# Kernel tuning notes

Hardware: AMD Instinct MI355X
Metric: run time of the kernel (lower is better)

The kernel has to match this reference:

```python
import jax, jax.numpy as jnp
import numpy as np
import math

HIDDEN = 384
HEADS = 4
HEAD_DIM = HIDDEN // HEADS
B, T = 8, 2048


def _shift_rel(pos_tensor):
    # pos_tensor: [b, h, t, 2t-1] -> [b, h, t, t] (Transformer-XL shift trick)
    b, h, t, n = pos_tensor.shape
    zero_pad = jnp.zeros((b, h, t, 1), dtype=pos_tensor.dtype)
    padded = jnp.concatenate([zero_pad, pos_tensor], axis=-1)  # [b,h,t,n+1]
    padded = padded.reshape(b, h, n + 1, t)
    shifted = padded[:, :, 1:].reshape(b, h, t, n)
    return shifted[:, :, :, : n // 2 + 1]  # [b,h,t,t]


def setup_inputs() -> dict:
    key = jax.random.key(0)
    ks = jax.random.split(key, 12)
    s = 1.0 / math.sqrt(HIDDEN)
    inp = {
        "hidden_states": jax.random.normal(ks[0], (B, T, HIDDEN), jnp.float32),
        "pos_emb": jax.random.normal(ks[1], (1, 2 * T - 1, HIDDEN), jnp.float32),
        "attention_mask": jnp.ones((B, 1, T), jnp.int32),
        "Wq": jax.random.normal(ks[2], (HIDDEN, HIDDEN), jnp.float32) * s,
        "bq": jnp.zeros((HIDDEN,), jnp.float32),
        "Wk": jax.random.normal(ks[3], (HIDDEN, HIDDEN), jnp.float32) * s,
        "bk": jnp.zeros((HIDDEN,), jnp.float32),
        "Wv": jax.random.normal(ks[4], (HIDDEN, HIDDEN), jnp.float32) * s,
        "bv": jnp.zeros((HIDDEN,), jnp.float32),
        "Wo": jax.random.normal(ks[5], (HIDDEN, HIDDEN), jnp.float32) * s,
        "bo": jnp.zeros((HIDDEN,), jnp.float32),
        "Wpos": jax.random.normal(ks[6], (HIDDEN, HIDDEN), jnp.float32) * s,
        "pos_bias_u": jax.random.normal(ks[7], (HEADS, HEAD_DIM), jnp.float32) * s,
        "pos_bias_v": jax.random.normal(ks[8], (HEADS, HEAD_DIM), jnp.float32) * s,
    }
    return inp


def reference(hidden_states, pos_emb, attention_mask, Wq, bq, Wk, bk, Wv, bv,
              Wo, bo, Wpos, pos_bias_u, pos_bias_v):
    bsz, q_len, _ = hidden_states.shape
    # projections (nn.Linear applies x @ W.T + b; weights here stored as [in, out])
    q = (hidden_states @ Wq + bq).reshape(bsz, q_len, HEADS, HEAD_DIM)
    k = (hidden_states @ Wk + bk).reshape(bsz, q_len, HEADS, HEAD_DIM)
    v = (hidden_states @ Wv + bv).reshape(bsz, q_len, HEADS, HEAD_DIM)
    pos = (pos_emb @ Wpos).reshape(pos_emb.shape[0], -1, HEADS, HEAD_DIM)

    q_u = (q + pos_bias_u).transpose(0, 2, 1, 3)  # [b,h,t,d]
    q_v = (q + pos_bias_v).transpose(0, 2, 1, 3)

    # content score: [b,h,t,t]
    matrix_ac = jnp.einsum('bhqd,bkhd->bhqk', q_u, k)
    # position score: [b,h,t,2t-1] then shift
    matrix_bd = jnp.einsum('bhqd,pnhd->bhqn', q_v, pos)
    matrix_bd = _shift_rel(matrix_bd)

    scores = (matrix_ac + matrix_bd) / math.sqrt(HEAD_DIM)

    mask = (attention_mask[:, None] == 0)  # [b,1,1,t]
    min_val = jnp.finfo(scores.dtype).min
    scores = jnp.where(mask, min_val, scores)
    attn = jax.nn.softmax(scores, axis=-1)
    attn = jnp.where(mask, 0.0, attn)

    out = jnp.einsum('bhqk,bkhd->bqhd', attn, v).reshape(bsz, q_len, HIDDEN)
    return out @ Wo + bo
```

## Files before the change

### kernel.cpp

```cpp
#include <hip/hip_runtime.h>
#include <hip/hip_bf16.h>

#define TSEQ 2048
#define HID 384
#define NHEAD 4
#define HD 96
#define NBATCH 8

using bf16 = __bf16;
typedef bf16 bf16x8 __attribute__((ext_vector_type(8)));
typedef bf16 bf16x4 __attribute__((ext_vector_type(4)));
typedef float f32x4 __attribute__((ext_vector_type(4)));
typedef unsigned long long u64;

static __device__ __forceinline__ f32x4 mfma16(bf16x8 a, bf16x8 b, f32x4 c) {
    return __builtin_amdgcn_mfma_f32_16x16x32_bf16(a, b, c, 0, 0, 0);
}

#define LDS_HANDOFF()                                   \
    __builtin_amdgcn_sched_barrier(0x7F);               \
    asm volatile("s_waitcnt lgkmcnt(0)");               \
    __builtin_amdgcn_sched_barrier(0x7F)

#define GL2LDS(g, l) __builtin_amdgcn_global_load_lds(                        \
    (const __attribute__((address_space(1))) unsigned int*)(const void*)(g),  \
    (__attribute__((address_space(3))) unsigned int*)(void*)(l), 16, 0, 0)

__global__ void k_conv8m(const float* __restrict__ hs, bf16* __restrict__ dhs,
                         const float* __restrict__ pe, bf16* __restrict__ dpe) {
    int blk = blockIdx.x;
    const float* src; bf16* dst; int t; int n8;
    if (blk < 3072) { src = hs; dst = dhs; t = blk * 256 + threadIdx.x; n8 = 786432; }
    else            { src = pe; dst = dpe; t = (blk - 3072) * 256 + threadIdx.x; n8 = 196560; }
    if (t >= n8) return;
    const float4* s4 = reinterpret_cast<const float4*>(src);
    float4 a = s4[2 * t], b = s4[2 * t + 1];
    bf16x8 o;
    o[0] = (bf16)a.x; o[1] = (bf16)a.y; o[2] = (bf16)a.z; o[3] = (bf16)a.w;
    o[4] = (bf16)b.x; o[5] = (bf16)b.y; o[6] = (bf16)b.z; o[7] = (bf16)b.w;
    *reinterpret_cast<bf16x8*>(dst + 8 * t) = o;
}

__global__ void k_convT5(const float* __restrict__ W0, const float* __restrict__ W1,
                         const float* __restrict__ W2, const float* __restrict__ W3,
                         const float* __restrict__ W4,
                         bf16* __restrict__ T0, bf16* __restrict__ T1,
                         bf16* __restrict__ T2, bf16* __restrict__ T3,
                         bf16* __restrict__ T4) {
    int t = blockIdx.x * 256 + threadIdx.x;
    int which = blockIdx.y;
    const float* W = (which == 0) ? W0 : (which == 1) ? W1 : (which == 2) ? W2
                     : (which == 3) ? W3 : W4;
    bf16* T = (which == 0) ? T0 : (which == 1) ? T1 : (which == 2) ? T2
              : (which == 3) ? T3 : T4;
    int n = t / HID, k = t % HID;
    T[t] = (bf16)W[(size_t)k * HID + n];
}

__launch_bounds__(256, 2)
__global__ void k_proj(const bf16* __restrict__ X, const bf16* __restrict__ P,
                       const bf16* __restrict__ wqT, const bf16* __restrict__ wkT,
                       const bf16* __restrict__ wvT, const bf16* __restrict__ wpT,
                       const float* __restrict__ bq, const float* __restrict__ bk,
                       const float* __restrict__ bv,
                       const float* __restrict__ pbu, const float* __restrict__ pbv,
                       bf16* __restrict__ qu, bf16* __restrict__ qv,
                       bf16* __restrict__ kws, bf16* __restrict__ vt,
                       bf16* __restrict__ pp) {
    __shared__ bf16 wt_lds[96][392];
    const float SC = 0.14724450f;
    int mat = blockIdx.z;
    int m0 = blockIdx.x * 64;
    if (mat == 3 && m0 >= 4095) return;
    int n0 = blockIdx.y * 96;
    const bf16* A  = (mat == 3) ? P : X;
    const bf16* WT = (mat == 0) ? wqT : (mat == 1) ? wkT : (mat == 2) ? wvT : wpT;
    int tid = threadIdx.x;
    #pragma unroll
    for (int s = 0; s < 18; ++s) {
        int cc = tid + 256 * s;
        int r = cc / 48, ch = cc % 48;
        *reinterpret_cast<int4*>(&wt_lds[r][ch * 8]) =
            *reinterpret_cast<const int4*>(WT + (size_t)(n0 + r) * HID + ch * 8);
    }
    __syncthreads();
    int lane = tid & 63, w = tid >> 6;
    int c = lane & 15, g = lane >> 4;
    int arow = m0 + 16 * w + c;
    if (mat == 3 && arow > 4095) arow = 4095;
    const bf16* Abase = A + (size_t)arow * HID + 8 * g;
    f32x4 acc[6] = {};
    for (int ks = 0; ks < 12; ++ks) {
        bf16x8 a = *reinterpret_cast<const bf16x8*>(Abase + 32 * ks);
        #pragma unroll
        for (int jt = 0; jt < 6; ++jt) {
            bf16x8 b = *reinterpret_cast<const bf16x8*>(&wt_lds[16 * jt + c][32 * ks + 8 * g]);
            acc[jt] = mfma16(a, b, acc[jt]);
        }
    }
    int h = blockIdx.y;
    int rbase = m0 + 16 * w + 4 * g;
    if (mat == 0) {
        #pragma unroll
        for (int jt = 0; jt < 6; ++jt) {
            int n = n0 + 16 * jt + c;
            int d = 16 * jt + c;
            float bb = bq[n], bu = pbu[n], bvv = pbv[n];
            #pragma unroll
            for (int j = 0; j < 4; ++j) {
                int m = rbase + j;
                int b_ = m >> 11, t = m & 2047;
                size_t o = (((size_t)(b_ * NHEAD + h)) * TSEQ + t) * HD + d;
                float q = acc[jt][j] + bb;
                qu[o] = (bf16)((q + bu) * SC);
                qv[o] = (bf16)((q + bvv) * SC);
            }
        }
    } else if (mat == 1) {
        #pragma unroll
        for (int jt = 0; jt < 6; ++jt) {
            int n = n0 + 16 * jt + c;
            int d = 16 * jt + c;
            float bb = bk[n];
            #pragma unroll
            for (int j = 0; j < 4; ++j) {
                int m = rbase + j;
                int b_ = m >> 11, t = m & 2047;
                size_t o = (((size_t)(b_ * NHEAD + h)) * TSEQ + t) * HD + d;
                kws[o] = (bf16)(acc[jt][j] + bb);
            }
        }
    } else if (mat == 2) {
        #pragma unroll
        for (int jt = 0; jt < 6; ++jt) {
            int d = 16 * jt + c;
            float bb = bv[n0 + 16 * jt + c];
            int m = rbase;
            int b_ = m >> 11, t0 = m & 2047;
            size_t o = (((size_t)(b_ * NHEAD + h)) * HD + d) * TSEQ + t0;
            bf16x4 pk;
            #pragma unroll
            for (int j = 0; j < 4; ++j) pk[j] = (bf16)(acc[jt][j] + bb);
            *reinterpret_cast<bf16x4*>(vt + o) = pk;
        }
    } else {
        #pragma unroll
        for (int jt = 0; jt < 6; ++jt) {
            int d = 16 * jt + c;
            #pragma unroll
            for (int j = 0; j < 4; ++j) {
                int m = rbase + j;
                if (m < 4095) {
                    size_t o = ((size_t)h * 4096 + m) * HD + d;
                    pp[o] = (bf16)acc[jt][j];
                }
            }
        }
    }
}

__launch_bounds__(256, 2)
__global__ void k_attn(const bf16* __restrict__ qu, const bf16* __restrict__ qv,
                       const bf16* __restrict__ kws, const bf16* __restrict__ vt,
                       const bf16* __restrict__ pp, const int* __restrict__ mask,
                       bf16* __restrict__ out) {
    __shared__ bf16 k_lds[128][104];
    __shared__ bf16 vt_lds[96][128];
    __shared__ bf16 wp_lds[4][16][168];

    int bid = blockIdx.x;
    int x = bid & 7, j5 = bid >> 3;
    int h = x & 3;
    int b_ = (x >> 2) * 4 + (j5 >> 5);
    int qb = j5 & 31;
    int bh = b_ * NHEAD + h;
    int q0 = qb * 64;

    int tid = threadIdx.x, lane = tid & 63, w = tid >> 6;
    int c = lane & 15, g = lane >> 4;
    const int NB = 2032 - q0 - 16 * w;

    bf16* k_flat = &k_lds[0][0];
    bf16* vt_flat = &vt_lds[0][0];
    int cc0 = tid, cc1 = tid + 256, cc2 = tid + 512, cc3 = tid + 768;
    int cc4 = tid + 1024, cc5 = tid + 1280, cc6 = tid + 1536;
    int kr0 = cc0 / 13, kc0 = cc0 % 13;  int kO0 = kr0 * HD + (kc0 == 12 ? 0 : kc0 * 8);
    int kr1 = cc1 / 13, kc1 = cc1 % 13;  int kO1 = kr1 * HD + (kc1 == 12 ? 0 : kc1 * 8);
    int kr2 = cc2 / 13, kc2 = cc2 % 13;  int kO2 = kr2 * HD + (kc2 == 12 ? 0 : kc2 * 8);
    int kr3 = cc3 / 13, kc3 = cc3 % 13;  int kO3 = kr3 * HD + (kc3 == 12 ? 0 : kc3 * 8);
    int kr4 = cc4 / 13, kc4 = cc4 % 13;  int kO4 = kr4 * HD + (kc4 == 12 ? 0 : kc4 * 8);
    int kr5 = cc5 / 13, kc5 = cc5 % 13;  int kO5 = kr5 * HD + (kc5 == 12 ? 0 : kc5 * 8);
    int kr6 = cc6 / 13, kc6 = cc6 % 13;  int kO6 = kr6 * HD + (kc6 == 12 ? 0 : kc6 * 8);
    bf16* kL0 = k_flat + (size_t)(64 * w + 0)    * 8;
    bf16* kL1 = k_flat + (size_t)(64 * w + 256)  * 8;
    bf16* kL2 = k_flat + (size_t)(64 * w + 512)  * 8;
    bf16* kL3 = k_flat + (size_t)(64 * w + 768)  * 8;
    bf16* kL4 = k_flat + (size_t)(64 * w + 1024) * 8;
    bf16* kL5 = k_flat + (size_t)(64 * w + 1280) * 8;
    bf16* kL6 = k_flat + (size_t)(64 * w + 1536) * 8;
    bool kAct6 = (w < 2);
    int vr0 = cc0 >> 4, vc0 = cc0 & 15;  int vO0 = vr0 * TSEQ + (vc0 ^ (vr0 & 7)) * 8;
    int vr1 = cc1 >> 4, vc1 = cc1 & 15;  int vO1 = vr1 * TSEQ + (vc1 ^ (vr1 & 7)) * 8;
    int vr2 = cc2 >> 4, vc2 = cc2 & 15;  int vO2 = vr2 * TSEQ + (vc2 ^ (vr2 & 7)) * 8;
    int vr3 = cc3 >> 4, vc3 = cc3 & 15;  int vO3 = vr3 * TSEQ + (vc3 ^ (vr3 & 7)) * 8;
    int vr4 = cc4 >> 4, vc4 = cc4 & 15;  int vO4 = vr4 * TSEQ + (vc4 ^ (vr4 & 7)) * 8;
    int vr5 = cc5 >> 4, vc5 = cc5 & 15;  int vO5 = vr5 * TSEQ + (vc5 ^ (vr5 & 7)) * 8;
    bf16* vL0 = vt_flat + (size_t)(64 * w + 0)    * 8;
    bf16* vL1 = vt_flat + (size_t)(64 * w + 256)  * 8;
    bf16* vL2 = vt_flat + (size_t)(64 * w + 512)  * 8;
    bf16* vL3 = vt_flat + (size_t)(64 * w + 768)  * 8;
    bf16* vL4 = vt_flat + (size_t)(64 * w + 1024) * 8;
    bf16* vL5 = vt_flat + (size_t)(64 * w + 1280) * 8;

    const bf16* kbP = kws + (size_t)bh * TSEQ * HD;
    const bf16* vbP = vt + (size_t)bh * HD * TSEQ;
    const bf16* pbP = pp + (size_t)h * 4096 * HD;
    const int*  mbP = mask + b_ * TSEQ;

    bf16x8 qu_f[3], qv_f[3];
    {
        size_t rowbase = ((size_t)bh * TSEQ + q0 + 16 * w + c) * HD + 8 * g;
        #pragma unroll
        for (int ds = 0; ds < 3; ++ds) {
            qu_f[ds] = *reinterpret_cast<const bf16x8*>(qu + rowbase + 32 * ds);
            qv_f[ds] = *reinterpret_cast<const bf16x8*>(qv + rowbase + 32 * ds);
        }
    }

    f32x4 acc_o[6] = {};
    float mrow = -3.0e38f, lrow = 0.f;
    f32x4 wc;
    int   mk0, mk1;

    bf16* wp_row = &wp_lds[w][c][0];
    const int hc = (15 - c) >> 2;
    const int sh = ((15 - c) & 3) * 16;

    auto winpair = [&](int wb, int ta, int tb) {
        f32x4 wa = {}, wbv = {};
        const bf16* pa = pbP + (size_t)(wb + 16 * ta + c) * HD + 8 * g;
        const bf16* pb = pbP + (size_t)(wb + 16 * tb + c) * HD + 8 * g;
        __builtin_amdgcn_s_setprio(1);
        #pragma unroll
        for (int ds = 0; ds < 3; ++ds) {
            wa  = mfma16(*reinterpret_cast<const bf16x8*>(pa + 32 * ds), qv_f[ds], wa);
            wbv = mfma16(*reinterpret_cast<const bf16x8*>(pb + 32 * ds), qv_f[ds], wbv);
        }
        __builtin_amdgcn_s_setprio(0);
        bf16x4 qa, qb;
        #pragma unroll
        for (int j = 0; j < 4; ++j) { qa[j] = (bf16)wa[j]; qb[j] = (bf16)wbv[j]; }
        *reinterpret_cast<bf16x4*>(wp_row + 16 * ta + 4 * g) = qa;
        *reinterpret_cast<bf16x4*>(wp_row + 16 * tb + 4 * g) = qb;
        return wbv;
    };

    {
        GL2LDS(kbP + kO0, kL0); GL2LDS(kbP + kO1, kL1); GL2LDS(kbP + kO2, kL2);
        GL2LDS(kbP + kO3, kL3); GL2LDS(kbP + kO4, kL4); GL2LDS(kbP + kO5, kL5);
        if (kAct6) GL2LDS(kbP + kO6, kL6);
        GL2LDS(vbP + vO0, vL0); GL2LDS(vbP + vO1, vL1); GL2LDS(vbP + vO2, vL2);
        GL2LDS(vbP + vO3, vL3); GL2LDS(vbP + vO4, vL4); GL2LDS(vbP + vO5, vL5);
        mk0 = mbP[lane]; mk1 = mbP[64 + lane];

        {
            f32x4 w0 = {};
            const bf16* p0 = pbP + (size_t)(NB + c) * HD + 8 * g;
            #pragma unroll
            for (int ds = 0; ds < 3; ++ds)
                w0 = mfma16(*reinterpret_cast<const bf16x8*>(p0 + 32 * ds), qv_f[ds], w0);
            bf16x4 q0v;
            #pragma unroll
            for (int j = 0; j < 4; ++j) q0v[j] = (bf16)w0[j];
            *reinterpret_cast<bf16x4*>(wp_row + 4 * g) = q0v;
        }
        winpair(NB, 1, 2);
        winpair(NB, 3, 4);
        winpair(NB, 5, 6);
        wc = winpair(NB, 7, 8);
    }
    __syncthreads();

    for (int kt = 0; kt < 16; ++kt) {
        unsigned long long bm0 = __ballot(mk0 != 0);
        unsigned long long bm1 = __ballot(mk1 != 0);

        bf16x4 wv[8];
        #pragma unroll
        for (int tk = 0; tk < 8; ++tk) {
            int qd = 4 * tk + g + hc;
            u64 A8 = *reinterpret_cast<const u64*>(wp_row + 4 * qd);
            u64 B8 = *reinterpret_cast<const u64*>(wp_row + 4 * qd + 4);
            u64 o8 = sh ? ((A8 >> sh) | (B8 << (64 - sh))) : A8;
            *reinterpret_cast<u64*>(&wv[tk]) = o8;
        }

        f32x4 acc_s[8];
        #pragma unroll
        for (int tk = 0; tk < 8; ++tk)
            acc_s[tk] = f32x4{(float)wv[tk][0], (float)wv[tk][1],
                              (float)wv[tk][2], (float)wv[tk][3]};
        __builtin_amdgcn_s_setprio(1);
        #pragma unroll
        for (int ds = 0; ds < 3; ++ds) {
            #pragma unroll
            for (int tk = 0; tk < 8; ++tk) {
                bf16x8 a = *reinterpret_cast<const bf16x8*>(
                    &k_lds[16 * tk + c][32 * ds + 8 * g]);
                acc_s[tk] = mfma16(a, qu_f[ds], acc_s[tk]);
            }
        }
        __builtin_amdgcn_s_setprio(0);

        if ((bm0 & bm1) != ~0ull) {
            #pragma unroll
            for (int tk = 0; tk < 8; ++tk) {
                unsigned long long bb = (tk < 4) ? bm0 : bm1;
                int base = 16 * (tk & 3) + 4 * g;
                #pragma unroll
                for (int j = 0; j < 4; ++j)
                    if (!((bb >> (base + j)) & 1)) acc_s[tk][j] = -3.0e38f;
            }
        }
        float pm = acc_s[0][0];
        #pragma unroll
        for (int tk = 0; tk < 8; ++tk)
            #pragma unroll
            for (int j = 0; j < 4; ++j) pm = fmaxf(pm, acc_s[tk][j]);
        pm = fmaxf(pm, __shfl_xor(pm, 16));
        pm = fmaxf(pm, __shfl_xor(pm, 32));
        if (!__all(pm <= mrow + 11.5415603f)) {
            float mnew = fmaxf(mrow, pm);
            float alpha = exp2f(mrow - mnew);
            mrow = mnew; lrow *= alpha;
            #pragma unroll
            for (int ot = 0; ot < 6; ++ot) acc_o[ot] *= alpha;
        }
        float rs = 0.f;
        #pragma unroll
        for (int tk = 0; tk < 8; ++tk)
            #pragma unroll
            for (int j = 0; j < 4; ++j) {
                float p = exp2f(acc_s[tk][j] - mrow);
                acc_s[tk][j] = p; rs += p;
            }
        rs += __shfl_xor(rs, 16);
        rs += __shfl_xor(rs, 32);
        lrow += rs;

        #pragma unroll
        for (int tk = 0; tk < 8; ++tk) {
            bf16x4 pk;
            #pragma unroll
            for (int j = 0; j < 4; ++j) pk[j] = (bf16)acc_s[tk][j];
            *reinterpret_cast<bf16x4*>(wp_row + 16 * tk + 4 * g) = pk;
        }
        LDS_HANDOFF();

        __builtin_amdgcn_s_setprio(1);
        #pragma unroll
        for (int ds = 0; ds < 4; ++ds) {
            bf16x8 pb_ = *reinterpret_cast<const bf16x8*>(wp_row + 32 * ds + 8 * g);
            #pragma unroll
            for (int ot = 0; ot < 6; ++ot) {
                int rr = 16 * ot + c;
                bf16x8 a = *reinterpret_cast<const bf16x8*>(
                    &vt_lds[rr][(((4 * ds + g) ^ (rr & 7)) * 8)]);
                acc_o[ot] = mfma16(a, pb_, acc_o[ot]);
            }
        }
        __builtin_amdgcn_s_setprio(0);

        if (kt < 15) {
            __syncthreads();

            int k0n = (kt + 1) * 128;
            const bf16* kb = kbP + (size_t)k0n * HD;
            const bf16* vb = vbP + k0n;
            GL2LDS(kb + kO0, kL0); GL2LDS(kb + kO1, kL1); GL2LDS(kb + kO2, kL2);
            GL2LDS(kb + kO3, kL3); GL2LDS(kb + kO4, kL4); GL2LDS(kb + kO5, kL5);
            if (kAct6) GL2LDS(kb + kO6, kL6);
            GL2LDS(vb + vO0, vL0); GL2LDS(vb + vO1, vL1); GL2LDS(vb + vO2, vL2);
            GL2LDS(vb + vO3, vL3); GL2LDS(vb + vO4, vL4); GL2LDS(vb + vO5, vL5);
            mk0 = mbP[k0n + lane]; mk1 = mbP[k0n + 64 + lane];

            int wb = NB + 128 * (kt + 1);
            bf16x4 q0v;
            #pragma unroll
            for (int j = 0; j < 4; ++j) q0v[j] = (bf16)wc[j];
            *reinterpret_cast<bf16x4*>(wp_row + 4 * g) = q0v;
            winpair(wb, 1, 2);
            winpair(wb, 3, 4);
            winpair(wb, 5, 6);
            wc = winpair(wb, 7, 8);

            __syncthreads();
        }
    }

    float inv = 1.0f / lrow;
    size_t m = (size_t)b_ * TSEQ + q0 + 16 * w + c;
    bf16* ob = out + m * HID + h * HD + 4 * g;
    #pragma unroll
    for (int ot = 0; ot < 6; ++ot) {
        bf16x4 pk;
        #pragma unroll
        for (int j = 0; j < 4; ++j) pk[j] = (bf16)(acc_o[ot][j] * inv);
        *reinterpret_cast<bf16x4*>(&ob[16 * ot]) = pk;
    }
}

__launch_bounds__(256, 2)
__global__ void k_oproj(const bf16* __restrict__ A, const bf16* __restrict__ WT,
                        const float* __restrict__ bias, float* __restrict__ out) {
    __shared__ bf16 wt_lds[96][392];
    int m0 = blockIdx.x * 64, n0 = blockIdx.y * 96;
    int tid = threadIdx.x;
    #pragma unroll
    for (int s = 0; s < 18; ++s) {
        int cc = tid + 256 * s;
        int r = cc / 48, ch = cc % 48;
        *reinterpret_cast<int4*>(&wt_lds[r][ch * 8]) =
            *reinterpret_cast<const int4*>(WT + (size_t)(n0 + r) * HID + ch * 8);
    }
    __syncthreads();
    int lane = tid & 63, w = tid >> 6;
    int c = lane & 15, g = lane >> 4;
    const bf16* Abase = A + (size_t)(m0 + 16 * w + c) * HID + 8 * g;
    f32x4 acc[6] = {};
    for (int ks = 0; ks < 12; ++ks) {
        bf16x8 a = *reinterpret_cast<const bf16x8*>(Abase + 32 * ks);
        #pragma unroll
        for (int jt = 0; jt < 6; ++jt) {
            bf16x8 b = *reinterpret_cast<const bf16x8*>(&wt_lds[16 * jt + c][32 * ks + 8 * g]);
            acc[jt] = mfma16(a, b, acc[jt]);
        }
    }
    int rbase = m0 + 16 * w + 4 * g;
    #pragma unroll
    for (int jt = 0; jt < 6; ++jt) {
        int n = n0 + 16 * jt + c;
        float bb = bias[n];
        #pragma unroll
        for (int j = 0; j < 4; ++j)
            out[(size_t)(rbase + j) * HID + n] = acc[jt][j] + bb;
    }
}

extern "C" void kernel_launch(void* const* d_in, const int* in_sizes, int n_in,
                              void* d_out, int out_size, void* d_ws, size_t ws_size,
                              hipStream_t stream) {
    const float* hs  = (const float*)d_in[0];
    const float* pe  = (const float*)d_in[1];
    const int*   msk = (const int*)d_in[2];
    const float* Wq  = (const float*)d_in[3];
    const float* bq  = (const float*)d_in[4];
    const float* Wk  = (const float*)d_in[5];
    const float* bk  = (const float*)d_in[6];
    const float* Wv  = (const float*)d_in[7];
    const float* bv  = (const float*)d_in[8];
    const float* Wo  = (const float*)d_in[9];
    const float* bo  = (const float*)d_in[10];
    const float* Wp  = (const float*)d_in[11];
    const float* pbu = (const float*)d_in[12];
    const float* pbv = (const float*)d_in[13];

    char* ws = (char*)d_ws;
    size_t off = 0;
    auto alloc = [&](size_t b) { char* p = ws + off; off += (b + 255) & ~(size_t)255; return p; };
    bf16* Xb  = (bf16*)alloc((size_t)16384 * HID * 2);
    bf16* Pb  = (bf16*)alloc((size_t)4096 * HID * 2);
    bf16* wqT = (bf16*)alloc((size_t)HID * HID * 2);
    bf16* wkT = (bf16*)alloc((size_t)HID * HID * 2);
    bf16* wvT = (bf16*)alloc((size_t)HID * HID * 2);
    bf16* woT = (bf16*)alloc((size_t)HID * HID * 2);
    bf16* wpT = (bf16*)alloc((size_t)HID * HID * 2);
    bf16* qu  = (bf16*)alloc((size_t)NBATCH * NHEAD * TSEQ * HD * 2);
    bf16* qv  = (bf16*)alloc((size_t)NBATCH * NHEAD * TSEQ * HD * 2);
    bf16* kws = (bf16*)alloc((size_t)NBATCH * NHEAD * TSEQ * HD * 2);
    bf16* vt  = (bf16*)alloc((size_t)NBATCH * NHEAD * TSEQ * HD * 2);
    bf16* pp  = (bf16*)alloc((size_t)NHEAD * 4096 * HD * 2 + 65536);
    bf16* ao  = (bf16*)alloc((size_t)16384 * HID * 2);

    k_conv8m<<<3840, 256, 0, stream>>>(hs, Xb, pe, Pb);
    k_convT5<<<dim3(576, 5), 256, 0, stream>>>(Wq, Wk, Wv, Wo, Wp,
                                               wqT, wkT, wvT, woT, wpT);
    k_proj<<<dim3(256, 4, 4), 256, 0, stream>>>(Xb, Pb, wqT, wkT, wvT, wpT,
                                                bq, bk, bv, pbu, pbv,
                                                qu, qv, kws, vt, pp);
    k_attn<<<1024, 256, 0, stream>>>(qu, qv, kws, vt, pp, msk, ao);
    k_oproj<<<dim3(256, 4), 256, 0, stream>>>(ao, woT, bo, (float*)d_out);
}
```

Baseline: 256.1 us.

## Double-buffer K/V tiles and use 512-thread blocks covering 128 queries in attention

The attention kernel now uses 8 waves per block, so each block covers 128 query rows and every K/V tile loaded into LDS is shared by twice as many queries. K and V tiles are double-buffered, and the next tile's global-to-LDS loads are issued at the start of each iteration so they overlap the current compute. This also removes one of the two barriers per iteration. In exchange, LDS use roughly doubles and there are half as many blocks (512), which may lower occupancy or leave some CUs idle.

```diff
diff --git a/kernel.cpp b/kernel.cpp
--- a/kernel.cpp
+++ b/kernel.cpp
@@ -159,58 +159,43 @@
     }
 }
 
-__launch_bounds__(256, 2)
+__launch_bounds__(512, 2)
 __global__ void k_attn(const bf16* __restrict__ qu, const bf16* __restrict__ qv,
                        const bf16* __restrict__ kws, const bf16* __restrict__ vt,
                        const bf16* __restrict__ pp, const int* __restrict__ mask,
                        bf16* __restrict__ out) {
-    __shared__ bf16 k_lds[128][104];
-    __shared__ bf16 vt_lds[96][128];
-    __shared__ bf16 wp_lds[4][16][168];
+    __shared__ bf16 kb0[128 * 104], kb1[128 * 104];
+    __shared__ bf16 vb0[96 * 128],  vb1[96 * 128];
+    __shared__ bf16 wp_lds[8][16][168];
 
     int bid = blockIdx.x;
-    int x = bid & 7, j5 = bid >> 3;
+    int x = bid & 7, j6 = bid >> 3;
     int h = x & 3;
-    int b_ = (x >> 2) * 4 + (j5 >> 5);
-    int qb = j5 & 31;
+    int b_ = (x >> 2) * 4 + (j6 >> 4);
+    int qb = j6 & 15;
     int bh = b_ * NHEAD + h;
-    int q0 = qb * 64;
+    int q0 = qb * 128;
 
     int tid = threadIdx.x, lane = tid & 63, w = tid >> 6;
     int c = lane & 15, g = lane >> 4;
     const int NB = 2032 - q0 - 16 * w;
 
-    bf16* k_flat = &k_lds[0][0];
-    bf16* vt_flat = &vt_lds[0][0];
-    int cc0 = tid, cc1 = tid + 256, cc2 = tid + 512, cc3 = tid + 768;
-    int cc4 = tid + 1024, cc5 = tid + 1280, cc6 = tid + 1536;
+    int cc0 = tid, cc1 = tid + 512, cc2 = tid + 1024, cc3 = tid + 1536;
     int kr0 = cc0 / 13, kc0 = cc0 % 13;  int kO0 = kr0 * HD + (kc0 == 12 ? 0 : kc0 * 8);
     int kr1 = cc1 / 13, kc1 = cc1 % 13;  int kO1 = kr1 * HD + (kc1 == 12 ? 0 : kc1 * 8);
     int kr2 = cc2 / 13, kc2 = cc2 % 13;  int kO2 = kr2 * HD + (kc2 == 12 ? 0 : kc2 * 8);
     int kr3 = cc3 / 13, kc3 = cc3 % 13;  int kO3 = kr3 * HD + (kc3 == 12 ? 0 : kc3 * 8);
-    int kr4 = cc4 / 13, kc4 = cc4 % 13;  int kO4 = kr4 * HD + (kc4 == 12 ? 0 : kc4 * 8);
-    int kr5 = cc5 / 13, kc5 = cc5 % 13;  int kO5 = kr5 * HD + (kc5 == 12 ? 0 : kc5 * 8);
-    int kr6 = cc6 / 13, kc6 = cc6 % 13;  int kO6 = kr6 * HD + (kc6 == 12 ? 0 : kc6 * 8);
-    bf16* kL0 = k_flat + (size_t)(64 * w + 0)    * 8;
-    bf16* kL1 = k_flat + (size_t)(64 * w + 256)  * 8;
-    bf16* kL2 = k_flat + (size_t)(64 * w + 512)  * 8;
-    bf16* kL3 = k_flat + (size_t)(64 * w + 768)  * 8;
-    bf16* kL4 = k_flat + (size_t)(64 * w + 1024) * 8;
-    bf16* kL5 = k_flat + (size_t)(64 * w + 1280) * 8;
-    bf16* kL6 = k_flat + (size_t)(64 * w + 1536) * 8;
-    bool kAct6 = (w < 2);
+    bool kAct3 = (w < 2);
+    size_t kD0 = (size_t)(64 * w + 0)    * 8;
+    size_t kD1 = (size_t)(64 * w + 512)  * 8;
+    size_t kD2 = (size_t)(64 * w + 1024) * 8;
+    size_t kD3 = (size_t)(64 * w + 1536) * 8;
     int vr0 = cc0 >> 4, vc0 = cc0 & 15;  int vO0 = vr0 * TSEQ + (vc0 ^ (vr0 & 7)) * 8;
     int vr1 = cc1 >> 4, vc1 = cc1 & 15;  int vO1 = vr1 * TSEQ + (vc1 ^ (vr1 & 7)) * 8;
     int vr2 = cc2 >> 4, vc2 = cc2 & 15;  int vO2 = vr2 * TSEQ + (vc2 ^ (vr2 & 7)) * 8;
-    int vr3 = cc3 >> 4, vc3 = cc3 & 15;  int vO3 = vr3 * TSEQ + (vc3 ^ (vr3 & 7)) * 8;
-    int vr4 = cc4 >> 4, vc4 = cc4 & 15;  int vO4 = vr4 * TSEQ + (vc4 ^ (vr4 & 7)) * 8;
-    int vr5 = cc5 >> 4, vc5 = cc5 & 15;  int vO5 = vr5 * TSEQ + (vc5 ^ (vr5 & 7)) * 8;
-    bf16* vL0 = vt_flat + (size_t)(64 * w + 0)    * 8;
-    bf16* vL1 = vt_flat + (size_t)(64 * w + 256)  * 8;
-    bf16* vL2 = vt_flat + (size_t)(64 * w + 512)  * 8;
-    bf16* vL3 = vt_flat + (size_t)(64 * w + 768)  * 8;
-    bf16* vL4 = vt_flat + (size_t)(64 * w + 1024) * 8;
-    bf16* vL5 = vt_flat + (size_t)(64 * w + 1280) * 8;
+    size_t vD0 = (size_t)(64 * w + 0)    * 8;
+    size_t vD1 = (size_t)(64 * w + 512)  * 8;
+    size_t vD2 = (size_t)(64 * w + 1024) * 8;
 
     const bf16* kbP = kws + (size_t)bh * TSEQ * HD;
     const bf16* vbP = vt + (size_t)bh * HD * TSEQ;
@@ -255,35 +240,21 @@
         return wbv;
     };
 
-    {
-        GL2LDS(kbP + kO0, kL0); GL2LDS(kbP + kO1, kL1); GL2LDS(kbP + kO2, kL2);
-        GL2LDS(kbP + kO3, kL3); GL2LDS(kbP + kO4, kL4); GL2LDS(kbP + kO5, kL5);
-        if (kAct6) GL2LDS(kbP + kO6, kL6);
-        GL2LDS(vbP + vO0, vL0); GL2LDS(vbP + vO1, vL1); GL2LDS(vbP + vO2, vL2);
-        GL2LDS(vbP + vO3, vL3); GL2LDS(vbP + vO4, vL4); GL2LDS(vbP + vO5, vL5);
-        mk0 = mbP[lane]; mk1 = mbP[64 + lane];
-
-        {
-            f32x4 w0 = {};
-            const bf16* p0 = pbP + (size_t)(NB + c) * HD + 8 * g;
-            #pragma unroll
-            for (int ds = 0; ds < 3; ++ds)
-                w0 = mfma16(*reinterpret_cast<const bf16x8*>(p0 + 32 * ds), qv_f[ds], w0);
-            bf16x4 q0v;
-            #pragma unroll
-            for (int j = 0; j < 4; ++j) q0v[j] = (bf16)w0[j];
-            *reinterpret_cast<bf16x4*>(wp_row + 4 * g) = q0v;
-        }
-        winpair(NB, 1, 2);
-        winpair(NB, 3, 4);
-        winpair(NB, 5, 6);
-        wc = winpair(NB, 7, 8);
-    }
-    __syncthreads();
-
-    for (int kt = 0; kt < 16; ++kt) {
-        unsigned long long bm0 = __ballot(mk0 != 0);
-        unsigned long long bm1 = __ballot(mk1 != 0);
+    auto iter = [&](int kt, bf16* krd, bf16* vrd, bf16* kwr, bf16* vwr) {
+        u64 bm0 = __ballot(mk0 != 0);
+        u64 bm1 = __ballot(mk1 != 0);
+        bool pre = kt < 15;
+        if (pre) {
+            int k0n = (kt + 1) * 128;
+            const bf16* kb = kbP + (size_t)k0n * HD;
+            const bf16* vb = vbP + k0n;
+            GL2LDS(kb + kO0, kwr + kD0); GL2LDS(kb + kO1, kwr + kD1);
+            GL2LDS(kb + kO2, kwr + kD2);
+            if (kAct3) GL2LDS(kb + kO3, kwr + kD3);
+            GL2LDS(vb + vO0, vwr + vD0); GL2LDS(vb + vO1, vwr + vD1);
+            GL2LDS(vb + vO2, vwr + vD2);
+            mk0 = mbP[k0n + lane]; mk1 = mbP[k0n + 64 + lane];
+        }
 
         bf16x4 wv[8];
         #pragma unroll
@@ -306,7 +277,7 @@
             #pragma unroll
             for (int tk = 0; tk < 8; ++tk) {
                 bf16x8 a = *reinterpret_cast<const bf16x8*>(
-                    &k_lds[16 * tk + c][32 * ds + 8 * g]);
+                    krd + (size_t)(16 * tk + c) * 104 + 32 * ds + 8 * g);
                 acc_s[tk] = mfma16(a, qu_f[ds], acc_s[tk]);
             }
         }
@@ -315,7 +286,7 @@
         if ((bm0 & bm1) != ~0ull) {
             #pragma unroll
             for (int tk = 0; tk < 8; ++tk) {
-                unsigned long long bb = (tk < 4) ? bm0 : bm1;
+                u64 bb = (tk < 4) ? bm0 : bm1;
                 int base = 16 * (tk & 3) + 4 * g;
                 #pragma unroll
                 for (int j = 0; j < 4; ++j)
@@ -365,25 +336,13 @@
             for (int ot = 0; ot < 6; ++ot) {
                 int rr = 16 * ot + c;
                 bf16x8 a = *reinterpret_cast<const bf16x8*>(
-                    &vt_lds[rr][(((4 * ds + g) ^ (rr & 7)) * 8)]);
+                    vrd + (size_t)rr * 128 + (((4 * ds + g) ^ (rr & 7)) * 8));
                 acc_o[ot] = mfma16(a, pb_, acc_o[ot]);
             }
         }
         __builtin_amdgcn_s_setprio(0);
 
-        if (kt < 15) {
-            __syncthreads();
-
-            int k0n = (kt + 1) * 128;
-            const bf16* kb = kbP + (size_t)k0n * HD;
-            const bf16* vb = vbP + k0n;
-            GL2LDS(kb + kO0, kL0); GL2LDS(kb + kO1, kL1); GL2LDS(kb + kO2, kL2);
-            GL2LDS(kb + kO3, kL3); GL2LDS(kb + kO4, kL4); GL2LDS(kb + kO5, kL5);
-            if (kAct6) GL2LDS(kb + kO6, kL6);
-            GL2LDS(vb + vO0, vL0); GL2LDS(vb + vO1, vL1); GL2LDS(vb + vO2, vL2);
-            GL2LDS(vb + vO3, vL3); GL2LDS(vb + vO4, vL4); GL2LDS(vb + vO5, vL5);
-            mk0 = mbP[k0n + lane]; mk1 = mbP[k0n + 64 + lane];
-
+        if (pre) {
             int wb = NB + 128 * (kt + 1);
             bf16x4 q0v;
             #pragma unroll
@@ -396,6 +355,37 @@
 
             __syncthreads();
         }
+    };
+
+    {
+        GL2LDS(kbP + kO0, kb0 + kD0); GL2LDS(kbP + kO1, kb0 + kD1);
+        GL2LDS(kbP + kO2, kb0 + kD2);
+        if (kAct3) GL2LDS(kbP + kO3, kb0 + kD3);
+        GL2LDS(vbP + vO0, vb0 + vD0); GL2LDS(vbP + vO1, vb0 + vD1);
+        GL2LDS(vbP + vO2, vb0 + vD2);
+        mk0 = mbP[lane]; mk1 = mbP[64 + lane];
+
+        {
+            f32x4 w0 = {};
+            const bf16* p0 = pbP + (size_t)(NB + c) * HD + 8 * g;
+            #pragma unroll
+            for (int ds = 0; ds < 3; ++ds)
+                w0 = mfma16(*reinterpret_cast<const bf16x8*>(p0 + 32 * ds), qv_f[ds], w0);
+            bf16x4 q0v;
+            #pragma unroll
+            for (int j = 0; j < 4; ++j) q0v[j] = (bf16)w0[j];
+            *reinterpret_cast<bf16x4*>(wp_row + 4 * g) = q0v;
+        }
+        winpair(NB, 1, 2);
+        winpair(NB, 3, 4);
+        winpair(NB, 5, 6);
+        wc = winpair(NB, 7, 8);
+    }
+    __syncthreads();
+
+    for (int kt2 = 0; kt2 < 16; kt2 += 2) {
+        iter(kt2,     kb0, vb0, kb1, vb1);
+        iter(kt2 + 1, kb1, vb1, kb0, vb0);
     }
 
     float inv = 1.0f / lrow;
@@ -488,6 +478,6 @@
     k_proj<<<dim3(256, 4, 4), 256, 0, stream>>>(Xb, Pb, wqT, wkT, wvT, wpT,
                                                 bq, bk, bv, pbu, pbv,
                                                 qu, qv, kws, vt, pp);
-    k_attn<<<1024, 256, 0, stream>>>(qu, qv, kws, vt, pp, msk, ao);
+    k_attn<<<512, 512, 0, stream>>>(qu, qv, kws, vt, pp, msk, ao);
     k_oproj<<<dim3(256, 4), 256, 0, stream>>>(ao, woT, bo, (float*)d_out);
 }
```

New measurement: 260.0 us. Within noise of the previous version (+1.5%).
